# Kernel tuning notes

Hardware: AMD Instinct MI355X
Metric: run time of the kernel (lower is better)

The kernel has to match this reference:

```python
import jax, jax.numpy as jnp
import numpy as np

HEADS = 4
DIM_HEAD = 128


def setup_inputs() -> dict:
    key = jax.random.key(0)
    k1, k2, k3, k4 = jax.random.split(key, 4)
    B, C, H, W = 8, 256, 64, 64
    hidden = HEADS * DIM_HEAD  # 512
    x = jax.random.normal(k1, (B, C, H, W), dtype=jnp.float32)
    # 1x1 convs are just channel matmuls; store kernels as [out_ch, in_ch]
    w_qkv = jax.random.normal(k2, (3 * hidden, C), dtype=jnp.float32) * 0.05
    w_out = jax.random.normal(k3, (C, hidden), dtype=jnp.float32) * 0.05
    b_out = jax.random.normal(k4, (C,), dtype=jnp.float32) * 0.05
    return {"x": x, "w_qkv": w_qkv, "w_out": w_out, "b_out": b_out}


def reference(x, w_qkv, w_out, b_out):
    B, C, H, W = x.shape
    n = H * W
    # to_qkv: 1x1 conv without bias == channel matmul
    qkv = jnp.einsum('bchw,oc->bohw', x, w_qkv)  # [B, 3*heads*dim_head, H, W]
    qkv = qkv.reshape(B, 3, HEADS, DIM_HEAD, n)  # 'b (qkv heads c) h w -> b qkv heads c n'
    q, k, v = qkv[:, 0], qkv[:, 1], qkv[:, 2]    # each [B, heads, dim_head, n]
    k = jax.nn.softmax(k, axis=-1)               # softmax over spatial positions
    context = jnp.einsum('bhdn,bhen->bhde', k, v)   # [B, heads, d, e]
    out = jnp.einsum('bhde,bhdn->bhen', context, q)  # [B, heads, e, n]
    out = out.reshape(B, HEADS * DIM_HEAD, H, W)
    # to_out: 1x1 conv with bias
    return jnp.einsum('bchw,oc->bohw', out, w_out) + b_out[None, :, None, None]
```

## Files before the change

kernel.cpp:

```cpp
#include <hip/hip_runtime.h>
#include <stdint.h>


using frag8 = __attribute__((ext_vector_type(8))) short;
using f32x4 = __attribute__((ext_vector_type(4))) float;

__device__ __forceinline__ float bf2f(unsigned short u) {
    union { unsigned int u; float f; } c;
    c.u = ((unsigned int)u) << 16;
    return c.f;
}
__device__ __forceinline__ unsigned short f2bf(float f) {
    union { float f; unsigned int u; } c; c.f = f;
    unsigned int u = c.u;
    return (unsigned short)((u + 0x7FFFu + ((u >> 16) & 1u)) >> 16);
}

__device__ __forceinline__ void gl_lds16(const void* g, void* l) {
    __builtin_amdgcn_global_load_lds(
        (const __attribute__((address_space(1))) unsigned int*)g,
        (__attribute__((address_space(3))) unsigned int*)l, 16, 0, 0);
}

__global__ __launch_bounds__(256) void k0_weights(
    const float* __restrict__ w_qkv, const float* __restrict__ w_out,
    unsigned short* __restrict__ wkvb, unsigned short* __restrict__ woutb,
    unsigned short* __restrict__ wqT)
{
    __shared__ float T[64][65];
    const int blk = blockIdx.x;
    const int tid = threadIdx.x;
    if (blk < 256) {
        const int idx = (blk * 256 + tid) * 4;
        float4 v = *(const float4*)(w_qkv + 512 * 256 + idx);
        ushort4 o;
        o.x = f2bf(v.x); o.y = f2bf(v.y); o.z = f2bf(v.z); o.w = f2bf(v.w);
        *(ushort4*)(wkvb + idx) = o;
    } else if (blk < 384) {
        const int idx = ((blk - 256) * 256 + tid) * 4;
        float4 v = *(const float4*)(w_out + idx);
        ushort4 o;
        o.x = f2bf(v.x); o.y = f2bf(v.y); o.z = f2bf(v.z); o.w = f2bf(v.w);
        *(ushort4*)(woutb + idx) = o;
    } else {
        const int t = blk - 384;
        const int j0 = (t >> 2) * 64, c0 = (t & 3) * 64;
        const int r = tid >> 4, cc = (tid & 15) * 4;
        #pragma unroll
        for (int p = 0; p < 4; ++p) {
            float4 v = *(const float4*)(w_qkv + (j0 + r + p * 16) * 256 + c0 + cc);
            T[r + p * 16][cc + 0] = v.x; T[r + p * 16][cc + 1] = v.y;
            T[r + p * 16][cc + 2] = v.z; T[r + p * 16][cc + 3] = v.w;
        }
        __syncthreads();
        const int c = tid >> 2, jj = (tid & 3) * 16;
        #pragma unroll
        for (int g = 0; g < 4; ++g) {
            ushort4 o;
            o.x = f2bf(T[jj + g * 4 + 0][c]);
            o.y = f2bf(T[jj + g * 4 + 1][c]);
            o.z = f2bf(T[jj + g * 4 + 2][c]);
            o.w = f2bf(T[jj + g * 4 + 3][c]);
            *(ushort4*)(wqT + (c0 + c) * 512 + j0 + jj + g * 4) = o;
        }
    }
}

__global__ __launch_bounds__(256) void k0_xt(
    const float* __restrict__ x, unsigned short* __restrict__ xbT)
{
    __shared__ float T[64][65];
    const int tid = threadIdx.x;
    const int n0 = blockIdx.x * 64, c0 = blockIdx.y * 64, b = blockIdx.z;
    const float* xb = x + (size_t)b * 1048576;
    const int cr = tid >> 4, nc = (tid & 15) * 4;
    #pragma unroll
    for (int p = 0; p < 4; ++p) {
        float4 v = *(const float4*)(xb + (size_t)(c0 + cr + p * 16) * 4096 + n0 + nc);
        T[cr + p * 16][nc + 0] = v.x; T[cr + p * 16][nc + 1] = v.y;
        T[cr + p * 16][nc + 2] = v.z; T[cr + p * 16][nc + 3] = v.w;
    }
    __syncthreads();
    const int n = tid >> 2, cc = (tid & 3) * 16;
    unsigned short* dst = xbT + (size_t)b * 1048576 + (size_t)(n0 + n) * 256 + c0 + cc;
    #pragma unroll
    for (int g = 0; g < 4; ++g) {
        ushort4 o;
        o.x = f2bf(T[cc + g * 4 + 0][n]);
        o.y = f2bf(T[cc + g * 4 + 1][n]);
        o.z = f2bf(T[cc + g * 4 + 2][n]);
        o.w = f2bf(T[cc + g * 4 + 3][n]);
        *(ushort4*)(dst + g * 4) = o;
    }
}

template<int MODE>
__global__ __launch_bounds__(256) void mfma_bt(
    const unsigned short* __restrict__ A0, int lda,
    const unsigned short* __restrict__ B0, int ldb,
    void* __restrict__ C0, int ldc,
    const float* __restrict__ bias, int Kp,
    unsigned long long sAz, unsigned long long sBz, unsigned long long sCz)
{
    __shared__ unsigned short As[128 * 32];
    __shared__ unsigned short Bs[128 * 32];
    const int tid  = threadIdx.x;
    const int w    = tid >> 6, lane = tid & 63;
    const int quad = lane >> 4, l16 = lane & 15;
    const int wm = (w >> 1) * 64, wn = (w & 1) * 64;
    const int z = blockIdx.z;

    const unsigned short* A;
    const unsigned short* B;
    int ks, ke, m0, n0;
    if constexpr (MODE == 2) {
        m0 = 0; n0 = 0;
        ks = blockIdx.x * 512; ke = ks + 512;
        const unsigned long long off =
            ((unsigned long long)(z >> 2) * 1024ull + (unsigned long long)(z & 3) * 128ull) * 4096ull;
        A = A0 + off; B = B0 + off;
    } else if constexpr (MODE == 3) {
        m0 = blockIdx.y * 128; n0 = 0;
        ks = 0; ke = Kp;
        A = A0 + (unsigned long long)(z & 3) * 128ull + (unsigned long long)m0 * lda;
        B = B0 + (unsigned long long)z * 16384ull;
    } else {
        m0 = blockIdx.y * 128; n0 = blockIdx.x * 128;
        ks = 0; ke = Kp;
        A = A0 + sAz * z + (unsigned long long)m0 * lda;
        B = B0 + sBz * z + (unsigned long long)n0 * ldb;
    }

    const int cA0 = w * 128 + lane;
    const int cA1 = cA0 + 64;
    const unsigned short* gA0 = A + (unsigned long long)(cA0 >> 2) * lda + (cA0 & 3) * 8;
    const unsigned short* gA1 = A + (unsigned long long)(cA1 >> 2) * lda + (cA1 & 3) * 8;
    const unsigned short* gB0 = B + (unsigned long long)(cA0 >> 2) * ldb + (cA0 & 3) * 8;
    const unsigned short* gB1 = B + (unsigned long long)(cA1 >> 2) * ldb + (cA1 & 3) * 8;
    unsigned short* lA0 = As + w * 1024;
    unsigned short* lA1 = As + w * 1024 + 512;
    unsigned short* lB0 = Bs + w * 1024;
    unsigned short* lB1 = Bs + w * 1024 + 512;

    f32x4 acc[4][4] = {};

    for (int k0 = ks; k0 < ke; k0 += 32) {
        gl_lds16(gA0 + k0, lA0);
        gl_lds16(gA1 + k0, lA1);
        gl_lds16(gB0 + k0, lB0);
        gl_lds16(gB1 + k0, lB1);
        __syncthreads();
        frag8 a[4], b[4];
        #pragma unroll
        for (int t = 0; t < 4; ++t) {
            a[t] = *(const frag8*)(As + (wm + t * 16 + l16) * 32 + quad * 8);
            b[t] = *(const frag8*)(Bs + (wn + t * 16 + l16) * 32 + quad * 8);
        }
        #pragma unroll
        for (int mt = 0; mt < 4; ++mt)
            #pragma unroll
            for (int nt = 0; nt < 4; ++nt)
                acc[mt][nt] = __builtin_amdgcn_mfma_f32_16x16x32_bf16(
                    a[mt], b[nt], acc[mt][nt], 0, 0, 0);
        __syncthreads();
    }

    if constexpr (MODE == 0 || MODE == 3) {
        unsigned short* C;
        if constexpr (MODE == 0)
            C = (unsigned short*)C0 + sCz * z + (unsigned long long)m0 * ldc + n0;
        else
            C = (unsigned short*)C0 + (unsigned long long)(z >> 2) * 131072ull
              + (unsigned long long)(z & 3) * 128ull + (unsigned long long)m0 * ldc;
        #pragma unroll
        for (int mt = 0; mt < 4; ++mt) {
            const int row = wm + mt * 16 + quad * 4;
            #pragma unroll
            for (int nt = 0; nt < 4; ++nt) {
                const int col = wn + nt * 16 + l16;
                #pragma unroll
                for (int r = 0; r < 4; ++r)
                    C[(unsigned long long)(row + r) * ldc + col] = f2bf(acc[mt][nt][r]);
            }
        }
    } else if constexpr (MODE == 1) {
        float* C = (float*)C0 + sCz * z + (unsigned long long)m0 * ldc + n0;
        const float* bp = bias + m0;
        #pragma unroll
        for (int mt = 0; mt < 4; ++mt) {
            const int row = wm + mt * 16 + quad * 4;
            #pragma unroll
            for (int nt = 0; nt < 4; ++nt) {
                const int col = wn + nt * 16 + l16;
                #pragma unroll
                for (int r = 0; r < 4; ++r)
                    C[(unsigned long long)(row + r) * ldc + col] = acc[mt][nt][r] + bp[row + r];
            }
        }
    } else {
        float* C = (float*)C0 + ((unsigned long long)blockIdx.x * 32 + z) * 16384ull;
        #pragma unroll
        for (int mt = 0; mt < 4; ++mt) {
            const int row = wm + mt * 16 + quad * 4;
            #pragma unroll
            for (int nt = 0; nt < 4; ++nt) {
                const int col = wn + nt * 16 + l16;
                #pragma unroll
                for (int r = 0; r < 4; ++r)
                    C[(row + r) * 128 + col] = acc[mt][nt][r];
            }
        }
    }
}

__global__ __launch_bounds__(256) void k2_softmax(unsigned short* __restrict__ kv)
{
    __shared__ float red[4];
    const int idx = blockIdx.x;
    const int b = idx >> 9, r = idx & 511;
    unsigned short* row = kv + (size_t)(b * 1024 + r) * 4096;
    const int tid = threadIdx.x;
    float v[16];
    #pragma unroll
    for (int g = 0; g < 4; ++g) {
        ushort4 u = *(const ushort4*)(row + g * 1024 + tid * 4);
        v[g * 4 + 0] = bf2f(u.x); v[g * 4 + 1] = bf2f(u.y);
        v[g * 4 + 2] = bf2f(u.z); v[g * 4 + 3] = bf2f(u.w);
    }
    float m = -1e30f;
    #pragma unroll
    for (int i = 0; i < 16; ++i) m = fmaxf(m, v[i]);
    #pragma unroll
    for (int off = 32; off > 0; off >>= 1) m = fmaxf(m, __shfl_down(m, off, 64));
    if ((tid & 63) == 0) red[tid >> 6] = m;
    __syncthreads();
    m = fmaxf(fmaxf(red[0], red[1]), fmaxf(red[2], red[3]));
    __syncthreads();
    float s = 0.f;
    #pragma unroll
    for (int i = 0; i < 16; ++i) { v[i] = __expf(v[i] - m); s += v[i]; }
    #pragma unroll
    for (int off = 32; off > 0; off >>= 1) s += __shfl_down(s, off, 64);
    if ((tid & 63) == 0) red[tid >> 6] = s;
    __syncthreads();
    s = red[0] + red[1] + red[2] + red[3];
    const float inv = 1.0f / s;
    #pragma unroll
    for (int g = 0; g < 4; ++g) {
        ushort4 u;
        u.x = f2bf(v[g * 4 + 0] * inv); u.y = f2bf(v[g * 4 + 1] * inv);
        u.z = f2bf(v[g * 4 + 2] * inv); u.w = f2bf(v[g * 4 + 3] * inv);
        *(ushort4*)(row + g * 1024 + tid * 4) = u;
    }
}

__global__ __launch_bounds__(256) void k3_sum(
    const float* __restrict__ ctxp, unsigned short* __restrict__ ctxb)
{
    const int idx = (blockIdx.x * 256 + threadIdx.x) * 4;
    float4 s = make_float4(0.f, 0.f, 0.f, 0.f);
    #pragma unroll
    for (int sl = 0; sl < 8; ++sl) {
        float4 t = *(const float4*)(ctxp + (size_t)sl * 524288 + idx);
        s.x += t.x; s.y += t.y; s.z += t.z; s.w += t.w;
    }
    ushort4 o;
    o.x = f2bf(s.x); o.y = f2bf(s.y); o.z = f2bf(s.z); o.w = f2bf(s.w);
    *(ushort4*)(ctxb + idx) = o;
}

extern "C" void kernel_launch(void* const* d_in, const int* in_sizes, int n_in,
                              void* d_out, int out_size, void* d_ws, size_t ws_size,
                              hipStream_t stream) {
    (void)in_sizes; (void)n_in; (void)out_size; (void)ws_size;
    const float* x     = (const float*)d_in[0];
    const float* w_qkv = (const float*)d_in[1];
    const float* w_out = (const float*)d_in[2];
    const float* b_out = (const float*)d_in[3];
    float* out = (float*)d_out;

    char* ws = (char*)d_ws;
    unsigned short* kv    = (unsigned short*)ws;
    unsigned short* xbT   = (unsigned short*)(ws + 67108864);
    unsigned short* wkvb  = (unsigned short*)(ws + 83886080);
    unsigned short* woutb = (unsigned short*)(ws + 84410368);
    unsigned short* wqT   = (unsigned short*)(ws + 84672512);
    float*          ctxp  = (float*)(ws + 84934656);
    unsigned short* ctxb  = (unsigned short*)(ws + 101711872);
    unsigned short* Mb    = (unsigned short*)(ws + 102760448);
    unsigned short* Nb    = (unsigned short*)(ws + 104857600);

    k0_weights<<<dim3(416), 256, 0, stream>>>(w_qkv, w_out, wkvb, woutb, wqT);
    k0_xt<<<dim3(64, 4, 8), 256, 0, stream>>>(x, xbT);
    mfma_bt<0><<<dim3(32, 8, 8), 256, 0, stream>>>(
        wkvb, 256, xbT, 256, kv, 4096, nullptr, 256,
        0ull, 1048576ull, 4194304ull);
    k2_softmax<<<dim3(4096), 256, 0, stream>>>(kv);
    mfma_bt<2><<<dim3(8, 1, 32), 256, 0, stream>>>(
        kv, 4096, kv + (size_t)512 * 4096, 4096, ctxp, 128, nullptr, 0,
        0ull, 0ull, 0ull);
    k3_sum<<<dim3(512), 256, 0, stream>>>(ctxp, ctxb);
    mfma_bt<3><<<dim3(1, 2, 32), 256, 0, stream>>>(
        woutb, 512, ctxb, 128, Mb, 512, nullptr, 128,
        0ull, 0ull, 0ull);
    mfma_bt<0><<<dim3(2, 2, 8), 256, 0, stream>>>(
        Mb, 512, wqT, 512, Nb, 256, nullptr, 512,
        131072ull, 0ull, 65536ull);
    mfma_bt<1><<<dim3(32, 2, 8), 256, 0, stream>>>(
        Nb, 256, xbT, 256, out, 4096, b_out, 256,
        65536ull, 1048576ull, 1048576ull);
}
```

Measured before the change: 184.5 us.

## Fold V projection into output weights; contract softmax(K) directly with x

Stops materialising V. The kernel now computes G = softmax(K)·xᵀ per head, over 256 input channels instead of 128 value dims, and folds W_v into the output weights through a precomputed U = W_out·W_vᵀ. The QKV projection GEMM now only produces K, which roughly halves the largest intermediate and its write/read traffic. In exchange it adds a row-major bf16 copy of x, a small weight GEMM, and a larger split-K context GEMM and reduction (256 columns instead of 128).

```diff
diff --git a/kernel.cpp b/kernel.cpp
--- a/kernel.cpp
+++ b/kernel.cpp
@@ -24,31 +24,35 @@
 
 __global__ __launch_bounds__(256) void k0_weights(
     const float* __restrict__ w_qkv, const float* __restrict__ w_out,
-    unsigned short* __restrict__ wkvb, unsigned short* __restrict__ woutb,
-    unsigned short* __restrict__ wqT)
+    unsigned short* __restrict__ wkb, unsigned short* __restrict__ woutb,
+    unsigned short* __restrict__ wqT, unsigned short* __restrict__ wvT)
 {
     __shared__ float T[64][65];
     const int blk = blockIdx.x;
     const int tid = threadIdx.x;
-    if (blk < 256) {
+    if (blk < 128) {
         const int idx = (blk * 256 + tid) * 4;
         float4 v = *(const float4*)(w_qkv + 512 * 256 + idx);
         ushort4 o;
         o.x = f2bf(v.x); o.y = f2bf(v.y); o.z = f2bf(v.z); o.w = f2bf(v.w);
-        *(ushort4*)(wkvb + idx) = o;
-    } else if (blk < 384) {
-        const int idx = ((blk - 256) * 256 + tid) * 4;
+        *(ushort4*)(wkb + idx) = o;
+    } else if (blk < 256) {
+        const int idx = ((blk - 128) * 256 + tid) * 4;
         float4 v = *(const float4*)(w_out + idx);
         ushort4 o;
         o.x = f2bf(v.x); o.y = f2bf(v.y); o.z = f2bf(v.z); o.w = f2bf(v.w);
         *(ushort4*)(woutb + idx) = o;
     } else {
-        const int t = blk - 384;
+        const int t2 = blk - 256;
+        const int which = t2 >> 5;
+        const int t = t2 & 31;
         const int j0 = (t >> 2) * 64, c0 = (t & 3) * 64;
+        const float* src = w_qkv + (which ? 1024 * 256 : 0);
+        unsigned short* dst = which ? wvT : wqT;
         const int r = tid >> 4, cc = (tid & 15) * 4;
         #pragma unroll
         for (int p = 0; p < 4; ++p) {
-            float4 v = *(const float4*)(w_qkv + (j0 + r + p * 16) * 256 + c0 + cc);
+            float4 v = *(const float4*)(src + (j0 + r + p * 16) * 256 + c0 + cc);
             T[r + p * 16][cc + 0] = v.x; T[r + p * 16][cc + 1] = v.y;
             T[r + p * 16][cc + 2] = v.z; T[r + p * 16][cc + 3] = v.w;
         }
@@ -61,13 +65,14 @@
             o.y = f2bf(T[jj + g * 4 + 1][c]);
             o.z = f2bf(T[jj + g * 4 + 2][c]);
             o.w = f2bf(T[jj + g * 4 + 3][c]);
-            *(ushort4*)(wqT + (c0 + c) * 512 + j0 + jj + g * 4) = o;
+            *(ushort4*)(dst + (c0 + c) * 512 + j0 + jj + g * 4) = o;
         }
     }
 }
 
 __global__ __launch_bounds__(256) void k0_xt(
-    const float* __restrict__ x, unsigned short* __restrict__ xbT)
+    const float* __restrict__ x, unsigned short* __restrict__ xbT,
+    unsigned short* __restrict__ xbc)
 {
     __shared__ float T[64][65];
     const int tid = threadIdx.x;
@@ -79,6 +84,9 @@
         float4 v = *(const float4*)(xb + (size_t)(c0 + cr + p * 16) * 4096 + n0 + nc);
         T[cr + p * 16][nc + 0] = v.x; T[cr + p * 16][nc + 1] = v.y;
         T[cr + p * 16][nc + 2] = v.z; T[cr + p * 16][nc + 3] = v.w;
+        ushort4 o;
+        o.x = f2bf(v.x); o.y = f2bf(v.y); o.z = f2bf(v.z); o.w = f2bf(v.w);
+        *(ushort4*)(xbc + (size_t)b * 1048576 + (size_t)(c0 + cr + p * 16) * 4096 + n0 + nc) = o;
     }
     __syncthreads();
     const int n = tid >> 2, cc = (tid & 3) * 16;
@@ -113,17 +121,16 @@
     const unsigned short* A;
     const unsigned short* B;
     int ks, ke, m0, n0;
-    if constexpr (MODE == 2) {
-        m0 = 0; n0 = 0;
-        ks = blockIdx.x * 512; ke = ks + 512;
-        const unsigned long long off =
-            ((unsigned long long)(z >> 2) * 1024ull + (unsigned long long)(z & 3) * 128ull) * 4096ull;
-        A = A0 + off; B = B0 + off;
-    } else if constexpr (MODE == 3) {
+    if constexpr (MODE == 3) {
         m0 = blockIdx.y * 128; n0 = 0;
-        ks = 0; ke = Kp;
-        A = A0 + (unsigned long long)(z & 3) * 128ull + (unsigned long long)m0 * lda;
-        B = B0 + (unsigned long long)z * 16384ull;
+        ks = 0; ke = 256;
+        A = A0 + (unsigned long long)(z & 3) * 65536ull + (unsigned long long)m0 * lda;
+        B = B0 + (unsigned long long)(z >> 2) * 131072ull + (unsigned long long)(z & 3) * 32768ull;
+    } else if constexpr (MODE == 4) {
+        m0 = blockIdx.y * 128; n0 = (blockIdx.x & 1) * 128;
+        ks = (blockIdx.x >> 1) * 1024; ke = ks + 1024;
+        A = A0 + sAz * z + (unsigned long long)m0 * lda;
+        B = B0 + sBz * z + (unsigned long long)n0 * ldb;
     } else {
         m0 = blockIdx.y * 128; n0 = blockIdx.x * 128;
         ks = 0; ke = Kp;
@@ -198,7 +205,8 @@
             }
         }
     } else {
-        float* C = (float*)C0 + ((unsigned long long)blockIdx.x * 32 + z) * 16384ull;
+        float* C = (float*)C0 + (unsigned long long)(blockIdx.x >> 1) * 1048576ull
+                 + sCz * z + (unsigned long long)m0 * ldc + n0;
         #pragma unroll
         for (int mt = 0; mt < 4; ++mt) {
             const int row = wm + mt * 16 + quad * 4;
@@ -207,18 +215,16 @@
                 const int col = wn + nt * 16 + l16;
                 #pragma unroll
                 for (int r = 0; r < 4; ++r)
-                    C[(row + r) * 128 + col] = acc[mt][nt][r];
+                    C[(unsigned long long)(row + r) * ldc + col] = acc[mt][nt][r];
             }
         }
     }
 }
 
-__global__ __launch_bounds__(256) void k2_softmax(unsigned short* __restrict__ kv)
+__global__ __launch_bounds__(256) void k2_softmax(unsigned short* __restrict__ Kb)
 {
     __shared__ float red[4];
-    const int idx = blockIdx.x;
-    const int b = idx >> 9, r = idx & 511;
-    unsigned short* row = kv + (size_t)(b * 1024 + r) * 4096;
+    unsigned short* row = Kb + (size_t)blockIdx.x * 4096;
     const int tid = threadIdx.x;
     float v[16];
     #pragma unroll
@@ -255,18 +261,18 @@
 }
 
 __global__ __launch_bounds__(256) void k3_sum(
-    const float* __restrict__ ctxp, unsigned short* __restrict__ ctxb)
+    const float* __restrict__ Gp, unsigned short* __restrict__ G)
 {
     const int idx = (blockIdx.x * 256 + threadIdx.x) * 4;
     float4 s = make_float4(0.f, 0.f, 0.f, 0.f);
     #pragma unroll
-    for (int sl = 0; sl < 8; ++sl) {
-        float4 t = *(const float4*)(ctxp + (size_t)sl * 524288 + idx);
+    for (int sl = 0; sl < 4; ++sl) {
+        float4 t = *(const float4*)(Gp + (size_t)sl * 1048576 + idx);
         s.x += t.x; s.y += t.y; s.z += t.z; s.w += t.w;
     }
     ushort4 o;
     o.x = f2bf(s.x); o.y = f2bf(s.y); o.z = f2bf(s.z); o.w = f2bf(s.w);
-    *(ushort4*)(ctxb + idx) = o;
+    *(ushort4*)(G + idx) = o;
 }
 
 extern "C" void kernel_launch(void* const* d_in, const int* in_sizes, int n_in,
@@ -280,28 +286,34 @@
     float* out = (float*)d_out;
 
     char* ws = (char*)d_ws;
-    unsigned short* kv    = (unsigned short*)ws;
-    unsigned short* xbT   = (unsigned short*)(ws + 67108864);
-    unsigned short* wkvb  = (unsigned short*)(ws + 83886080);
-    unsigned short* woutb = (unsigned short*)(ws + 84410368);
-    unsigned short* wqT   = (unsigned short*)(ws + 84672512);
-    float*          ctxp  = (float*)(ws + 84934656);
-    unsigned short* ctxb  = (unsigned short*)(ws + 101711872);
-    unsigned short* Mb    = (unsigned short*)(ws + 102760448);
-    unsigned short* Nb    = (unsigned short*)(ws + 104857600);
-
-    k0_weights<<<dim3(416), 256, 0, stream>>>(w_qkv, w_out, wkvb, woutb, wqT);
-    k0_xt<<<dim3(64, 4, 8), 256, 0, stream>>>(x, xbT);
-    mfma_bt<0><<<dim3(32, 8, 8), 256, 0, stream>>>(
-        wkvb, 256, xbT, 256, kv, 4096, nullptr, 256,
-        0ull, 1048576ull, 4194304ull);
-    k2_softmax<<<dim3(4096), 256, 0, stream>>>(kv);
-    mfma_bt<2><<<dim3(8, 1, 32), 256, 0, stream>>>(
-        kv, 4096, kv + (size_t)512 * 4096, 4096, ctxp, 128, nullptr, 0,
-        0ull, 0ull, 0ull);
-    k3_sum<<<dim3(512), 256, 0, stream>>>(ctxp, ctxb);
+    unsigned short* Kb    = (unsigned short*)ws;
+    unsigned short* xbT   = (unsigned short*)(ws + 33554432);
+    unsigned short* xbc   = (unsigned short*)(ws + 50331648);
+    unsigned short* wkb   = (unsigned short*)(ws + 67108864);
+    unsigned short* woutb = (unsigned short*)(ws + 67371008);
+    unsigned short* wqT   = (unsigned short*)(ws + 67633152);
+    unsigned short* wvT   = (unsigned short*)(ws + 67895296);
+    unsigned short* U     = (unsigned short*)(ws + 68157440);
+    float*          Gp    = (float*)(ws + 68681728);
+    unsigned short* G     = (unsigned short*)(ws + 85458944);
+    unsigned short* Mb    = (unsigned short*)(ws + 87556096);
+    unsigned short* Nb    = (unsigned short*)(ws + 89653248);
+
+    k0_weights<<<dim3(320), 256, 0, stream>>>(w_qkv, w_out, wkb, woutb, wqT, wvT);
+    mfma_bt<0><<<dim3(2, 2, 4), 256, 0, stream>>>(
+        woutb, 512, wvT, 512, U, 256, nullptr, 128,
+        128ull, 128ull, 65536ull);
+    k0_xt<<<dim3(64, 4, 8), 256, 0, stream>>>(x, xbT, xbc);
+    mfma_bt<0><<<dim3(32, 4, 8), 256, 0, stream>>>(
+        wkb, 256, xbT, 256, Kb, 4096, nullptr, 256,
+        0ull, 1048576ull, 2097152ull);
+    k2_softmax<<<dim3(4096), 256, 0, stream>>>(Kb);
+    mfma_bt<4><<<dim3(8, 4, 8), 256, 0, stream>>>(
+        Kb, 4096, xbc, 4096, Gp, 256, nullptr, 0,
+        2097152ull, 1048576ull, 131072ull);
+    k3_sum<<<dim3(1024), 256, 0, stream>>>(Gp, G);
     mfma_bt<3><<<dim3(1, 2, 32), 256, 0, stream>>>(
-        woutb, 512, ctxb, 128, Mb, 512, nullptr, 128,
+        U, 256, G, 256, Mb, 512, nullptr, 256,
         0ull, 0ull, 0ull);
     mfma_bt<0><<<dim3(2, 2, 8), 256, 0, stream>>>(
         Mb, 512, wqT, 512, Nb, 256, nullptr, 512,
```

After: 194.5 us. 5.4% more time.
